# Performance work log

Measured on AMD Instinct MI355X. Metric: run time of the kernel, lower is better.

The kernel has to match this reference:

```python
import jax, jax.numpy as jnp
import numpy as np

B, L = 4096, 4096
HID = 16  # hidden width of the tiny per-digit adder MLP


def setup_inputs() -> dict:
    key = jax.random.key(0)
    k1, k2, k3, k4, k5, k6 = jax.random.split(key, 6)
    return {
        "x1": jax.random.uniform(k1, (B, L), dtype=jnp.float32),
        "x2": jax.random.uniform(k2, (B, L), dtype=jnp.float32),
        "W1": jax.random.normal(k3, (3, HID), dtype=jnp.float32),
        "b1": jax.random.normal(k4, (HID,), dtype=jnp.float32),
        "W2": jax.random.normal(k5, (HID, 2), dtype=jnp.float32),
        "b2": jax.random.normal(k6, (2,), dtype=jnp.float32),
    }


def reference(x1, x2, W1, b1, W2, b2):
    # Sequential digit-wise adder: scan over the length axis carrying c.
    def step(c, cols):
        a, b = cols  # each [B]
        inp = jnp.stack([a, b, c], axis=-1)          # [B, 3]
        h = jax.nn.relu(inp @ W1 + b1)               # [B, HID]
        out = jax.nn.sigmoid(h @ W2 + b2)            # [B, 2] -> (sum_bit, carry)
        return out[:, 1], out[:, 0]

    c0 = jnp.zeros((x1.shape[0],), dtype=x1.dtype)
    c_final, ys = jax.lax.scan(step, c0, (x1.T, x2.T))  # ys: [L, B]
    return ys.T, c_final[:, None]
```

## Files before the change

### kernel.cpp

```cpp
#include <hip/hip_runtime.h>


#define HIDDEN 16
constexpr int Bn = 4096;
constexpr int Ln = 4096;
constexpr int CHUNK = 128;
constexpr int WARM = 48;
constexpr int NCHUNK = Ln / CHUNK;
constexpr int GRAN = 16;

__device__ __forceinline__ float fast_exp2(float x) {
#if __has_builtin(__builtin_amdgcn_exp2f)
  return __builtin_amdgcn_exp2f(x);
#else
  return exp2f(x);
#endif
}
__device__ __forceinline__ float fast_rcp(float x) {
#if __has_builtin(__builtin_amdgcn_rcpf)
  return __builtin_amdgcn_rcpf(x);
#else
  return 1.0f / x;
#endif
}
__device__ __forceinline__ float sigmoid_pre(float z) {
  return fast_rcp(1.0f + fast_exp2(z));
}

__global__ __launch_bounds__(64) void seq_adder_kernel(
    const float* __restrict__ x1, const float* __restrict__ x2,
    const float* __restrict__ W1, const float* __restrict__ b1,
    const float* __restrict__ W2, const float* __restrict__ b2,
    float* __restrict__ out) {
  const int row = blockIdx.x * 64 + threadIdx.x;
  const int ci = blockIdx.y;

  constexpr float NLOG2E = -1.4426950408889634f;

  float w1a[HIDDEN], w1b[HIDDEN], w1c[HIDDEN], bb1[HIDDEN];
  float w2s[HIDDEN], w2c[HIDDEN];
#pragma unroll
  for (int j = 0; j < HIDDEN; ++j) {
    w1a[j] = W1[j];
    w1b[j] = W1[HIDDEN + j];
    w1c[j] = W1[2 * HIDDEN + j];
    bb1[j] = b1[j];
    w2s[j] = W2[2 * j + 0] * NLOG2E;
    w2c[j] = W2[2 * j + 1] * NLOG2E;
  }
  const float b2s = b2[0] * NLOG2E, b2c = b2[1] * NLOG2E;

  const float* __restrict__ r1 = x1 + (size_t)row * Ln;
  const float* __restrict__ r2 = x2 + (size_t)row * Ln;
  float* __restrict__ yo = out + (size_t)row * Ln;

  const int l0 = ci * CHUNK;
  float c;

  if (ci == 0) {
    c = 0.0f;
  } else {
    c = 0.5f;
    for (int g = 0; g < WARM / GRAN; ++g) {
      const int lb = l0 - WARM + g * GRAN;
      float4 a4[GRAN / 4], b4[GRAN / 4];
#pragma unroll
      for (int q = 0; q < GRAN / 4; ++q) {
        a4[q] = *reinterpret_cast<const float4*>(r1 + lb + 4 * q);
        b4[q] = *reinterpret_cast<const float4*>(r2 + lb + 4 * q);
      }
      const float* af = reinterpret_cast<const float*>(a4);
      const float* bf = reinterpret_cast<const float*>(b4);
#pragma unroll
      for (int u = 0; u < GRAN; ++u) {
        const float a = af[u];
        const float b = bf[u];
        float pre[HIDDEN];
#pragma unroll
        for (int j = 0; j < HIDDEN; ++j)
          pre[j] = fmaf(a, w1a[j], fmaf(b, w1b[j], bb1[j]));
        float zc0 = b2c, zc1 = 0.f, zc2 = 0.f, zc3 = 0.f;
#pragma unroll
        for (int j = 0; j < HIDDEN; j += 4) {
          float h0 = fmaxf(fmaf(c, w1c[j + 0], pre[j + 0]), 0.f);
          float h1 = fmaxf(fmaf(c, w1c[j + 1], pre[j + 1]), 0.f);
          float h2 = fmaxf(fmaf(c, w1c[j + 2], pre[j + 2]), 0.f);
          float h3 = fmaxf(fmaf(c, w1c[j + 3], pre[j + 3]), 0.f);
          zc0 = fmaf(h0, w2c[j + 0], zc0);
          zc1 = fmaf(h1, w2c[j + 1], zc1);
          zc2 = fmaf(h2, w2c[j + 2], zc2);
          zc3 = fmaf(h3, w2c[j + 3], zc3);
        }
        c = sigmoid_pre((zc0 + zc1) + (zc2 + zc3));
      }
    }
  }

  for (int g = 0; g < CHUNK / GRAN; ++g) {
    const int lb = l0 + g * GRAN;
    float4 a4[GRAN / 4], b4[GRAN / 4], y4[GRAN / 4];
#pragma unroll
    for (int q = 0; q < GRAN / 4; ++q) {
      a4[q] = *reinterpret_cast<const float4*>(r1 + lb + 4 * q);
      b4[q] = *reinterpret_cast<const float4*>(r2 + lb + 4 * q);
    }
    const float* af = reinterpret_cast<const float*>(a4);
    const float* bf = reinterpret_cast<const float*>(b4);
    float* yf = reinterpret_cast<float*>(y4);
#pragma unroll
    for (int u = 0; u < GRAN; ++u) {
      const float a = af[u];
      const float b = bf[u];
      float pre[HIDDEN];
#pragma unroll
      for (int j = 0; j < HIDDEN; ++j)
        pre[j] = fmaf(a, w1a[j], fmaf(b, w1b[j], bb1[j]));
      float zc0 = b2c, zc1 = 0.f, zc2 = 0.f, zc3 = 0.f;
      float zs0 = b2s, zs1 = 0.f;
#pragma unroll
      for (int j = 0; j < HIDDEN; j += 4) {
        float h0 = fmaxf(fmaf(c, w1c[j + 0], pre[j + 0]), 0.f);
        float h1 = fmaxf(fmaf(c, w1c[j + 1], pre[j + 1]), 0.f);
        float h2 = fmaxf(fmaf(c, w1c[j + 2], pre[j + 2]), 0.f);
        float h3 = fmaxf(fmaf(c, w1c[j + 3], pre[j + 3]), 0.f);
        zc0 = fmaf(h0, w2c[j + 0], zc0);
        zc1 = fmaf(h1, w2c[j + 1], zc1);
        zc2 = fmaf(h2, w2c[j + 2], zc2);
        zc3 = fmaf(h3, w2c[j + 3], zc3);
        zs0 = fmaf(h0, w2s[j + 0], fmaf(h1, w2s[j + 1], zs0));
        zs1 = fmaf(h2, w2s[j + 2], fmaf(h3, w2s[j + 3], zs1));
      }
      yf[u] = sigmoid_pre(zs0 + zs1);
      c = sigmoid_pre((zc0 + zc1) + (zc2 + zc3));
    }
#pragma unroll
    for (int q = 0; q < GRAN / 4; ++q) {
      *reinterpret_cast<float4*>(yo + lb + 4 * q) = y4[q];
    }
  }

  if (ci == NCHUNK - 1) {
    out[(size_t)Bn * Ln + row] = c;
  }
}

extern "C" void kernel_launch(void* const* d_in, const int* in_sizes, int n_in,
                              void* d_out, int out_size, void* d_ws,
                              size_t ws_size, hipStream_t stream) {
  const float* x1 = (const float*)d_in[0];
  const float* x2 = (const float*)d_in[1];
  const float* W1 = (const float*)d_in[2];
  const float* b1 = (const float*)d_in[3];
  const float* W2 = (const float*)d_in[4];
  const float* b2 = (const float*)d_in[5];
  float* out = (float*)d_out;

  dim3 grid(Bn / 64, NCHUNK);
  seq_adder_kernel<<<grid, 64, 0, stream>>>(x1, x2, W1, b1, W2, b2, out);
}
```

Before: 83.61 us.

## Stage input tiles through LDS with coalesced loads and register prefetch

Each wavefront now loads 64x16 input tiles cooperatively, with four lanes covering one row's 16 contiguous floats. It writes them into padded shared-memory tiles and each lane reads back its own row. The next tile is prefetched into registers while the current one is computed, so global load latency overlaps the serial MLP recurrence. This adds shared-memory traffic and register pressure. No barrier is used because the block is a single 64-thread wavefront, and that correctness relies on lockstep execution within the wave.

```diff
diff --git a/kernel.cpp b/kernel.cpp
--- a/kernel.cpp
+++ b/kernel.cpp
@@ -8,6 +8,9 @@
 constexpr int WARM = 48;
 constexpr int NCHUNK = Ln / CHUNK;
 constexpr int GRAN = 16;
+constexpr int WG = WARM / GRAN;
+constexpr int MG = CHUNK / GRAN;
+constexpr int LSTR = 20;
 
 __device__ __forceinline__ float fast_exp2(float x) {
 #if __has_builtin(__builtin_amdgcn_exp2f)
@@ -32,7 +35,9 @@
     const float* __restrict__ W1, const float* __restrict__ b1,
     const float* __restrict__ W2, const float* __restrict__ b2,
     float* __restrict__ out) {
-  const int row = blockIdx.x * 64 + threadIdx.x;
+  const int l = threadIdx.x;
+  const int rowbase = blockIdx.x * 64;
+  const int row = rowbase + l;
   const int ci = blockIdx.y;
 
   constexpr float NLOG2E = -1.4426950408889634f;
@@ -50,25 +55,64 @@
   }
   const float b2s = b2[0] * NLOG2E, b2c = b2[1] * NLOG2E;
 
-  const float* __restrict__ r1 = x1 + (size_t)row * Ln;
-  const float* __restrict__ r2 = x2 + (size_t)row * Ln;
+  __shared__ float lds_a[64 * LSTR];
+  __shared__ float lds_b[64 * LSTR];
+
   float* __restrict__ yo = out + (size_t)row * Ln;
+
+  const int cr = l >> 2;
+  const int cc = (l & 3) * 4;
+  const float* ga = x1 + (size_t)(rowbase + cr) * Ln + cc;
+  const float* gb = x2 + (size_t)(rowbase + cr) * Ln + cc;
 
   const int l0 = ci * CHUNK;
   float c;
 
+  float4 va[4], vb[4];
+
+#define LOAD_TILE(lb)                                                     \
+  do {                                                                    \
+    _Pragma("unroll") for (int i_ = 0; i_ < 4; ++i_) {                    \
+      va[i_] = *reinterpret_cast<const float4*>(ga + (size_t)i_ * 16 * Ln \
+                                                + (lb));                  \
+      vb[i_] = *reinterpret_cast<const float4*>(gb + (size_t)i_ * 16 * Ln \
+                                                + (lb));                  \
+    }                                                                     \
+  } while (0)
+
+#define STORE_LDS()                                                          \
+  do {                                                                       \
+    _Pragma("unroll") for (int i_ = 0; i_ < 4; ++i_) {                       \
+      *reinterpret_cast<float4*>(&lds_a[(i_ * 16 + cr) * LSTR + cc]) =       \
+          va[i_];                                                            \
+      *reinterpret_cast<float4*>(&lds_b[(i_ * 16 + cr) * LSTR + cc]) =       \
+          vb[i_];                                                            \
+    }                                                                        \
+  } while (0)
+
+#define READ_LDS(a4, b4)                                                    \
+  do {                                                                      \
+    _Pragma("unroll") for (int q_ = 0; q_ < 4; ++q_) {                      \
+      (a4)[q_] =                                                            \
+          *reinterpret_cast<const float4*>(&lds_a[l * LSTR + q_ * 4]);      \
+      (b4)[q_] =                                                            \
+          *reinterpret_cast<const float4*>(&lds_b[l * LSTR + q_ * 4]);      \
+    }                                                                       \
+  } while (0)
+
   if (ci == 0) {
     c = 0.0f;
+    LOAD_TILE(l0);
   } else {
     c = 0.5f;
-    for (int g = 0; g < WARM / GRAN; ++g) {
-      const int lb = l0 - WARM + g * GRAN;
-      float4 a4[GRAN / 4], b4[GRAN / 4];
-#pragma unroll
-      for (int q = 0; q < GRAN / 4; ++q) {
-        a4[q] = *reinterpret_cast<const float4*>(r1 + lb + 4 * q);
-        b4[q] = *reinterpret_cast<const float4*>(r2 + lb + 4 * q);
-      }
+    const int w0 = l0 - WARM;
+    LOAD_TILE(w0);
+#pragma unroll 1
+    for (int t = 0; t < WG; ++t) {
+      STORE_LDS();
+      float4 a4[4], b4[4];
+      READ_LDS(a4, b4);
+      LOAD_TILE(w0 + (t + 1) * GRAN);
       const float* af = reinterpret_cast<const float*>(a4);
       const float* bf = reinterpret_cast<const float*>(b4);
 #pragma unroll
@@ -96,14 +140,12 @@
     }
   }
 
-  for (int g = 0; g < CHUNK / GRAN; ++g) {
-    const int lb = l0 + g * GRAN;
-    float4 a4[GRAN / 4], b4[GRAN / 4], y4[GRAN / 4];
-#pragma unroll
-    for (int q = 0; q < GRAN / 4; ++q) {
-      a4[q] = *reinterpret_cast<const float4*>(r1 + lb + 4 * q);
-      b4[q] = *reinterpret_cast<const float4*>(r2 + lb + 4 * q);
-    }
+#pragma unroll 1
+  for (int g = 0; g < MG; ++g) {
+    STORE_LDS();
+    float4 a4[4], b4[4], y4[4];
+    READ_LDS(a4, b4);
+    if (g + 1 < MG) LOAD_TILE(l0 + (g + 1) * GRAN);
     const float* af = reinterpret_cast<const float*>(a4);
     const float* bf = reinterpret_cast<const float*>(b4);
     float* yf = reinterpret_cast<float*>(y4);
@@ -134,8 +176,8 @@
       c = sigmoid_pre((zc0 + zc1) + (zc2 + zc3));
     }
 #pragma unroll
-    for (int q = 0; q < GRAN / 4; ++q) {
-      *reinterpret_cast<float4*>(yo + lb + 4 * q) = y4[q];
+    for (int q = 0; q < 4; ++q) {
+      *reinterpret_cast<float4*>(yo + l0 + g * GRAN + 4 * q) = y4[q];
     }
   }
 
```

After: 127.5 us. 52.5% more time.
